# Kernel optimization log

Hardware: AMD Instinct MI355X
Metric: run time of the kernel (lower is better)

Reference implementation:

```python
import jax, jax.numpy as jnp
import numpy as np

ZMAX = 92          # max atomic number in NLH table
BOHR = 0.52917721  # Bohr radius in Angstrom (au.BOHR)
ENERGY_UNIT = 1.0  # multiplier for 'Ha'
N_ATOMS = 100_000
N_EDGES = 6_400_000
TAB = (ZMAX + 1) ** 2  # 8649


def setup_inputs() -> dict:
    key = jax.random.key(0)
    k1, k2, k3, k4, k5, k6, k7 = jax.random.split(key, 7)
    species = jax.random.randint(k1, (N_ATOMS,), 0, 93, dtype=jnp.int32)
    edge_src = jax.random.randint(k2, (N_EDGES,), 0, N_ATOMS, dtype=jnp.int32)
    edge_dst = jax.random.randint(k3, (N_EDGES,), 0, N_ATOMS, dtype=jnp.int32)
    # distances kept away from zero (division by rijs)
    distances = 0.5 + 4.5 * jax.random.uniform(k4, (N_EDGES,), dtype=jnp.float32)
    switch = jax.random.uniform(k5, (N_EDGES,), dtype=jnp.float32)
    CS = jax.random.uniform(k6, (TAB, 3), dtype=jnp.float32)
    ALPHAS = jax.random.uniform(k7, (TAB, 3), dtype=jnp.float32) + 0.5
    return {"species": species, "edge_src": edge_src, "edge_dst": edge_dst,
            "distances": distances, "switch": switch, "CS": CS, "ALPHAS": ALPHAS}


def reference(species, edge_src, edge_dst, distances, switch, CS, ALPHAS):
    # pair index into (zmax+1)^2 coefficient table
    s12 = species[edge_src] + ZMAX * species[edge_dst]
    cs = CS[s12]          # [E, 3]
    alphas = ALPHAS[s12]  # [E, 3]
    Z = jnp.where(species > 0, species.astype(distances.dtype), 0.0)
    # 3-term exponential screening function
    phi = jnp.sum(cs * jnp.exp(-alphas * distances[:, None]), axis=-1)  # [E]
    ereppair = Z[edge_src] * Z[edge_dst] * phi * switch / distances
    erep_atomic = ENERGY_UNIT * 0.5 * BOHR * jax.ops.segment_sum(
        ereppair, edge_src, num_segments=species.shape[0])
    return erep_atomic
```

## Files before the change

### kernel.cpp

```cpp
#include <hip/hip_runtime.h>
#include <hip/hip_fp16.h>


#define ZMAX_C 92
#define TAB93  93
#define NTAB   (TAB93 * TAB93)
#define HALF_BOHR 0.264588605f
#define NBMAX 64
#define APB 2048
#define APB_LOG 11
#define SPLITS 16
#define TPB 256
#define EPT 16
#define BLK_EDGES (TPB * EPT)

typedef int            ivec4 __attribute__((ext_vector_type(4)));
typedef float          fvec4 __attribute__((ext_vector_type(4)));

#if __has_builtin(__builtin_amdgcn_rcpf)
#define FAST_RCP(x) __builtin_amdgcn_rcpf(x)
#else
#define FAST_RCP(x) (1.0f / (x))
#endif

__global__ __launch_bounds__(TPB) void p0_prep(
    const float* __restrict__ CS, const float* __restrict__ ALPHAS,
    const int* __restrict__ species,
    uint4* __restrict__ tab16, unsigned char* __restrict__ spc8,
    unsigned* __restrict__ cursor, int n_atoms, int nb)
{
    int i = blockIdx.x * TPB + threadIdx.x;
    if (i < NTAB) {
        int sd = i / TAB93;
        int ss = i - TAB93 * sd;
        int ref = ss + ZMAX_C * sd;
        float Z = (ss > 0 && sd > 0) ? (float)(ss * sd) : 0.0f;
        __half h[8];
        h[0] = __float2half_rn(CS[3*ref+0] * Z);
        h[1] = __float2half_rn(CS[3*ref+1] * Z);
        h[2] = __float2half_rn(CS[3*ref+2] * Z);
        h[3] = __float2half_rn(-ALPHAS[3*ref+0]);
        h[4] = __float2half_rn(-ALPHAS[3*ref+1]);
        h[5] = __float2half_rn(-ALPHAS[3*ref+2]);
        h[6] = __half(0.0f); h[7] = __half(0.0f);
        tab16[i] = *reinterpret_cast<uint4*>(h);
    }
    if (i < n_atoms) spc8[i] = (unsigned char)species[i];
    if (i < nb) cursor[i] = 0u;
}

__device__ __forceinline__ float half_lo(unsigned u) {
    return __half2float(*reinterpret_cast<const __half*>(&u));
}
__device__ __forceinline__ float half_hi(unsigned u) {
    unsigned s = u >> 16;
    return __half2float(*reinterpret_cast<const __half*>(&s));
}

__global__ __launch_bounds__(TPB) void p1_bin(
    const int* __restrict__ edge_src, const int* __restrict__ edge_dst,
    const float* __restrict__ dist, const float* __restrict__ swt,
    const unsigned char* __restrict__ spc8, const uint4* __restrict__ tab16,
    unsigned* __restrict__ pairs, unsigned* __restrict__ cursor,
    int nb, int cap, int n_edges)
{
    __shared__ unsigned stage[BLK_EDGES];
    __shared__ unsigned hist4[4][NBMAX];
    __shared__ unsigned hist[NBMAX];
    __shared__ unsigned lbase[NBMAX];
    __shared__ unsigned gbase[NBMAX];

    int tid = threadIdx.x;
    if (tid < NBMAX) {
        hist4[0][tid] = 0; hist4[1][tid] = 0;
        hist4[2][tid] = 0; hist4[3][tid] = 0;
    }
    __syncthreads();

    int lane = tid & 63, wave = tid >> 6;
    long long wbase = (long long)blockIdx.x * BLK_EDGES + (long long)wave * (64 * EPT);

    unsigned meta[EPT];
    unsigned short s12r[EPT];

    {
        int srcv[EPT], dstv[EPT];
        #pragma unroll
        for (int j = 0; j < EPT / 4; ++j) {
            long long e0 = wbase + j * 256 + lane * 4;
            if (e0 + 3 < (long long)n_edges) {
                ivec4 s4 = __builtin_nontemporal_load((const ivec4*)(edge_src + e0));
                ivec4 d4 = __builtin_nontemporal_load((const ivec4*)(edge_dst + e0));
                #pragma unroll
                for (int k = 0; k < 4; ++k) { srcv[j*4+k] = s4[k]; dstv[j*4+k] = d4[k]; }
            } else {
                #pragma unroll
                for (int k = 0; k < 4; ++k) {
                    long long e = e0 + k;
                    bool v = (e < (long long)n_edges);
                    srcv[j*4+k] = v ? edge_src[e] : 0;
                    dstv[j*4+k] = v ? edge_dst[e] : 0;
                }
            }
        }
        int ssv[EPT], sdv[EPT];
        #pragma unroll
        for (int i = 0; i < EPT; ++i) ssv[i] = spc8[srcv[i]];
        #pragma unroll
        for (int i = 0; i < EPT; ++i) sdv[i] = spc8[dstv[i]];
        #pragma unroll
        for (int j = 0; j < EPT / 4; ++j) {
            long long e0 = wbase + j * 256 + lane * 4;
            #pragma unroll
            for (int k = 0; k < 4; ++k) {
                int idx = j * 4 + k;
                s12r[idx] = (unsigned short)(ssv[idx] + TAB93 * sdv[idx]);
                meta[idx] = 0u;
                if (e0 + k < (long long)n_edges) {
                    unsigned b    = (unsigned)srcv[idx] >> APB_LOG;
                    unsigned lsrc = (unsigned)srcv[idx] & (APB - 1);
                    unsigned rank = atomicAdd(&hist4[wave][b], 1u);
                    meta[idx] = 0x80000000u | (rank << 17) | (b << 11) | lsrc;
                }
            }
        }
    }
    __syncthreads();
    if (tid < 64) {
        unsigned h0 = hist4[0][tid], h1 = hist4[1][tid];
        unsigned h2 = hist4[2][tid], h3 = hist4[3][tid];
        unsigned tot = h0 + h1 + h2 + h3;
        hist4[0][tid] = 0;
        hist4[1][tid] = h0;
        hist4[2][tid] = h0 + h1;
        hist4[3][tid] = h0 + h1 + h2;
        if (tid < nb) hist[tid] = tot;
        unsigned v = (tid < nb) ? tot : 0u;
        unsigned x = v;
        #pragma unroll
        for (int off = 1; off < 64; off <<= 1) {
            unsigned y = __shfl_up(x, off);
            if ((tid & 63) >= off) x += y;
        }
        if (tid < nb) {
            lbase[tid] = x - v;
            gbase[tid] = v ? atomicAdd(cursor + tid, v) : 0u;
        }
    }
    __syncthreads();

    for (int jj = 0; jj < EPT / 8; ++jj) {
        long long eA = wbase + (jj*2+0) * 256 + lane * 4;
        long long eB = wbase + (jj*2+1) * 256 + lane * 4;
        float rA[4], wA[4], rB[4], wB[4];
        bool fullB = (eB + 3 < (long long)n_edges);
        if (fullB) {
            fvec4 r4 = __builtin_nontemporal_load((const fvec4*)(dist + eA));
            fvec4 w4 = __builtin_nontemporal_load((const fvec4*)(swt + eA));
            fvec4 r5 = __builtin_nontemporal_load((const fvec4*)(dist + eB));
            fvec4 w5 = __builtin_nontemporal_load((const fvec4*)(swt + eB));
            #pragma unroll
            for (int k = 0; k < 4; ++k) {
                rA[k] = r4[k]; wA[k] = w4[k]; rB[k] = r5[k]; wB[k] = w5[k];
            }
        } else {
            #pragma unroll
            for (int k = 0; k < 4; ++k) {
                long long ea = eA + k, eb = eB + k;
                bool va = (ea < (long long)n_edges), vb = (eb < (long long)n_edges);
                rA[k] = va ? dist[ea] : 1.f;  wA[k] = va ? swt[ea] : 0.f;
                rB[k] = vb ? dist[eb] : 1.f;  wB[k] = vb ? swt[eb] : 0.f;
            }
        }
        uint4 tA[4], tB[4];
        #pragma unroll
        for (int k = 0; k < 4; ++k) tA[k] = tab16[s12r[jj*8 + k]];
        #pragma unroll
        for (int k = 0; k < 4; ++k) tB[k] = tab16[s12r[jj*8 + 4 + k]];
        #pragma unroll
        for (int g = 0; g < 2; ++g) {
            const float* r = g ? rB : rA;
            const float* w = g ? wB : wA;
            const uint4* t = g ? tB : tA;
            #pragma unroll
            for (int k = 0; k < 4; ++k) {
                int idx = jj * 8 + g * 4 + k;
                unsigned m = meta[idx];
                if (!(m & 0x80000000u)) continue;
                float c0 = half_lo(t[k].x), c1 = half_hi(t[k].x);
                float c2 = half_lo(t[k].y), na0 = half_hi(t[k].y);
                float na1 = half_lo(t[k].z), na2 = half_hi(t[k].z);
                float phi = c0 * __expf(na0 * r[k])
                          + c1 * __expf(na1 * r[k])
                          + c2 * __expf(na2 * r[k]);
                float val = HALF_BOHR * phi * w[k] * FAST_RCP(r[k]);
                unsigned b = (m >> 11) & 63u;
                unsigned pos = lbase[b] + hist4[wave][b] + ((m >> 17) & 0x3FFFu);
                unsigned short hb = __half_as_ushort(__float2half_rn(val));
                stage[pos] = ((m & (APB - 1)) << 16) | (unsigned)hb;
            }
        }
    }
    __syncthreads();
    for (int b = wave; b < nb; b += 4) {
        unsigned cnt = hist[b], lb = lbase[b], gb = gbase[b];
        unsigned* dst = pairs + (size_t)b * (size_t)cap + gb;
        for (unsigned i = lane; i < cnt; i += 64)
            if (gb + i < (unsigned)cap) dst[i] = stage[lb + i];
    }
}

__global__ __launch_bounds__(TPB) void p2a_reduce(
    const unsigned* __restrict__ pairs, const unsigned* __restrict__ cursor,
    float* __restrict__ partial, int cap, int stride)
{
    int b = blockIdx.x / SPLITS;
    int s = blockIdx.x % SPLITS;
    __shared__ float acc[APB];
    for (int i = threadIdx.x; i < APB; i += TPB) acc[i] = 0.f;
    __syncthreads();
    unsigned cnt = cursor[b];
    if (cnt > (unsigned)cap) cnt = (unsigned)cap;
    unsigned nq = (cnt + 3u) >> 2;
    unsigned qb = (unsigned)((unsigned long long)nq * s / SPLITS);
    unsigned qe = (unsigned)((unsigned long long)nq * (s + 1) / SPLITS);
    const uint4* p4 = (const uint4*)(pairs + (size_t)b * (size_t)cap);
    for (unsigned q = qb + threadIdx.x; q < qe; q += TPB) {
        uint4 v = p4[q];
        unsigned base = q << 2;
        if (base + 3u < cnt) {
            unsafeAtomicAdd(&acc[v.x >> 16], __half2float(__ushort_as_half((unsigned short)(v.x & 0xFFFFu))));
            unsafeAtomicAdd(&acc[v.y >> 16], __half2float(__ushort_as_half((unsigned short)(v.y & 0xFFFFu))));
            unsafeAtomicAdd(&acc[v.z >> 16], __half2float(__ushort_as_half((unsigned short)(v.z & 0xFFFFu))));
            unsafeAtomicAdd(&acc[v.w >> 16], __half2float(__ushort_as_half((unsigned short)(v.w & 0xFFFFu))));
        } else {
            unsigned vv[4] = {v.x, v.y, v.z, v.w};
            #pragma unroll
            for (int e = 0; e < 4; ++e)
                if (base + (unsigned)e < cnt)
                    unsafeAtomicAdd(&acc[vv[e] >> 16],
                        __half2float(__ushort_as_half((unsigned short)(vv[e] & 0xFFFFu))));
        }
    }
    __syncthreads();
    float* prow = partial + (size_t)s * stride + (size_t)b * APB;
    for (int k = threadIdx.x; k < APB; k += TPB) prow[k] = acc[k];
}

__global__ __launch_bounds__(TPB) void p2b_sum(
    const float* __restrict__ partial, float* __restrict__ out, int n, int stride)
{
    int i = blockIdx.x * TPB + threadIdx.x;
    if (i >= n) return;
    float s = 0.f;
    #pragma unroll
    for (int x = 0; x < SPLITS; ++x) s += partial[(size_t)x * stride + i];
    out[i] = s;
}

__global__ __launch_bounds__(TPB) void erep_edges_direct(
    const int* __restrict__ edge_src, const int* __restrict__ edge_dst,
    const float* __restrict__ dist, const float* __restrict__ swt,
    const int* __restrict__ species, const float* __restrict__ CS,
    const float* __restrict__ ALPHAS, float* __restrict__ out, int n_edges)
{
    int e = blockIdx.x * TPB + threadIdx.x;
    if (e >= n_edges) return;
    int ss = species[edge_src[e]], sd = species[edge_dst[e]];
    int prod = ss * sd;
    if (prod == 0) return;
    int s12 = ss + ZMAX_C * sd;
    float r = dist[e];
    float phi = CS[3*s12+0] * __expf(-ALPHAS[3*s12+0] * r)
              + CS[3*s12+1] * __expf(-ALPHAS[3*s12+1] * r)
              + CS[3*s12+2] * __expf(-ALPHAS[3*s12+2] * r);
    atomicAdd(out + edge_src[e],
              HALF_BOHR * (float)prod * phi * swt[e] * FAST_RCP(r));
}

extern "C" void kernel_launch(void* const* d_in, const int* in_sizes, int n_in,
                              void* d_out, int out_size, void* d_ws, size_t ws_size,
                              hipStream_t stream)
{
    const int*   species  = (const int*)  d_in[0];
    const int*   edge_src = (const int*)  d_in[1];
    const int*   edge_dst = (const int*)  d_in[2];
    const float* dist     = (const float*)d_in[3];
    const float* swt      = (const float*)d_in[4];
    const float* CS       = (const float*)d_in[5];
    const float* ALPHAS   = (const float*)d_in[6];
    float* out = (float*)d_out;

    int n_atoms = in_sizes[0];
    int n_edges = in_sizes[1];

    int nb = (n_atoms + APB - 1) / APB;
    long long capll = (long long)n_edges / nb + (long long)n_edges / ((long long)nb * 32) + 256;
    int cap = (int)((capll + 31) & ~31LL);
    int stride = nb * APB;

    size_t pairs_sz = ((size_t)nb * (size_t)cap * 4 + 255) & ~(size_t)255;
    size_t cur_sz   = ((size_t)nb * 4 + 255) & ~(size_t)255;
    size_t part_sz  = ((size_t)SPLITS * (size_t)stride * 4 + 255) & ~(size_t)255;
    size_t tab_sz   = ((size_t)NTAB * 16 + 255) & ~(size_t)255;
    size_t spc_sz   = ((size_t)n_atoms + 255) & ~(size_t)255;
    size_t need = pairs_sz + cur_sz + part_sz + tab_sz + spc_sz;

    if (nb <= NBMAX && n_edges > 0 && ws_size >= need) {
        char* w = (char*)d_ws;
        unsigned*       pairs   = (unsigned*)w;
        unsigned*       cursor  = (unsigned*)(w + pairs_sz);
        float*          partial = (float*)(w + pairs_sz + cur_sz);
        uint4*          tab16   = (uint4*)(w + pairs_sz + cur_sz + part_sz);
        unsigned char*  spc8    = (unsigned char*)(w + pairs_sz + cur_sz + part_sz + tab_sz);

        int pmax = n_atoms > NTAB ? n_atoms : NTAB;
        p0_prep<<<(pmax + TPB - 1) / TPB, TPB, 0, stream>>>(
            CS, ALPHAS, species, tab16, spc8, cursor, n_atoms, nb);

        p1_bin<<<(n_edges + BLK_EDGES - 1) / BLK_EDGES, TPB, 0, stream>>>(
            edge_src, edge_dst, dist, swt, spc8, tab16,
            pairs, cursor, nb, cap, n_edges);

        p2a_reduce<<<nb * SPLITS, TPB, 0, stream>>>(pairs, cursor, partial, cap, stride);
        p2b_sum<<<(n_atoms + TPB - 1) / TPB, TPB, 0, stream>>>(partial, out, n_atoms, stride);
    } else {
        (void)hipMemsetAsync(d_out, 0, (size_t)out_size * sizeof(float), stream);
        erep_edges_direct<<<(n_edges + TPB - 1) / TPB, TPB, 0, stream>>>(
            edge_src, edge_dst, dist, swt, species, CS, ALPHAS, out, n_edges);
    }
}
```

Before: 249.0 us.

## Drop partial-sum kernel, atomically reduce into output, halve edges per thread

The separate p2b_sum pass and the SPLITS-row partial buffer are removed. Each p2a_reduce block now atomically adds its nonzero shared-memory accumulators straight into the output, which p0_prep zeroes first. EPT is also halved from 16 to 8, so p1_bin launches twice as many blocks, and the nontemporal loads become ordinary vector loads. This saves one launch and the partial-buffer traffic, but adds global float atomics (16-way contention per atom) and makes the summation order nondeterministic.

New measurement: 241.1 us. 1.03x faster.

```diff
diff --git a/kernel.cpp b/kernel.cpp
--- a/kernel.cpp
+++ b/kernel.cpp
@@ -11,7 +11,7 @@
 #define APB_LOG 11
 #define SPLITS 16
 #define TPB 256
-#define EPT 16
+#define EPT 8
 #define BLK_EDGES (TPB * EPT)
 
 typedef int            ivec4 __attribute__((ext_vector_type(4)));
@@ -27,7 +27,8 @@
     const float* __restrict__ CS, const float* __restrict__ ALPHAS,
     const int* __restrict__ species,
     uint4* __restrict__ tab16, unsigned char* __restrict__ spc8,
-    unsigned* __restrict__ cursor, int n_atoms, int nb)
+    unsigned* __restrict__ cursor, float* __restrict__ out,
+    int n_atoms, int nb)
 {
     int i = blockIdx.x * TPB + threadIdx.x;
     if (i < NTAB) {
@@ -45,7 +46,10 @@
         h[6] = __half(0.0f); h[7] = __half(0.0f);
         tab16[i] = *reinterpret_cast<uint4*>(h);
     }
-    if (i < n_atoms) spc8[i] = (unsigned char)species[i];
+    if (i < n_atoms) {
+        spc8[i] = (unsigned char)species[i];
+        out[i] = 0.0f;
+    }
     if (i < nb) cursor[i] = 0u;
 }
 
@@ -89,8 +93,8 @@
         for (int j = 0; j < EPT / 4; ++j) {
             long long e0 = wbase + j * 256 + lane * 4;
             if (e0 + 3 < (long long)n_edges) {
-                ivec4 s4 = __builtin_nontemporal_load((const ivec4*)(edge_src + e0));
-                ivec4 d4 = __builtin_nontemporal_load((const ivec4*)(edge_dst + e0));
+                ivec4 s4 = *reinterpret_cast<const ivec4*>(edge_src + e0);
+                ivec4 d4 = *reinterpret_cast<const ivec4*>(edge_dst + e0);
                 #pragma unroll
                 for (int k = 0; k < 4; ++k) { srcv[j*4+k] = s4[k]; dstv[j*4+k] = d4[k]; }
             } else {
@@ -155,10 +159,10 @@
         float rA[4], wA[4], rB[4], wB[4];
         bool fullB = (eB + 3 < (long long)n_edges);
         if (fullB) {
-            fvec4 r4 = __builtin_nontemporal_load((const fvec4*)(dist + eA));
-            fvec4 w4 = __builtin_nontemporal_load((const fvec4*)(swt + eA));
-            fvec4 r5 = __builtin_nontemporal_load((const fvec4*)(dist + eB));
-            fvec4 w5 = __builtin_nontemporal_load((const fvec4*)(swt + eB));
+            fvec4 r4 = *reinterpret_cast<const fvec4*>(dist + eA);
+            fvec4 w4 = *reinterpret_cast<const fvec4*>(swt + eA);
+            fvec4 r5 = *reinterpret_cast<const fvec4*>(dist + eB);
+            fvec4 w5 = *reinterpret_cast<const fvec4*>(swt + eB);
             #pragma unroll
             for (int k = 0; k < 4; ++k) {
                 rA[k] = r4[k]; wA[k] = w4[k]; rB[k] = r5[k]; wB[k] = w5[k];
@@ -212,7 +216,7 @@
 
 __global__ __launch_bounds__(TPB) void p2a_reduce(
     const unsigned* __restrict__ pairs, const unsigned* __restrict__ cursor,
-    float* __restrict__ partial, int cap, int stride)
+    float* __restrict__ out, int cap, int n_atoms)
 {
     int b = blockIdx.x / SPLITS;
     int s = blockIdx.x % SPLITS;
@@ -243,19 +247,13 @@
         }
     }
     __syncthreads();
-    float* prow = partial + (size_t)s * stride + (size_t)b * APB;
-    for (int k = threadIdx.x; k < APB; k += TPB) prow[k] = acc[k];
-}
-
-__global__ __launch_bounds__(TPB) void p2b_sum(
-    const float* __restrict__ partial, float* __restrict__ out, int n, int stride)
-{
-    int i = blockIdx.x * TPB + threadIdx.x;
-    if (i >= n) return;
-    float s = 0.f;
-    #pragma unroll
-    for (int x = 0; x < SPLITS; ++x) s += partial[(size_t)x * stride + i];
-    out[i] = s;
+    int abase = b * APB;
+    for (int k = threadIdx.x; k < APB; k += TPB) {
+        int atom = abase + k;
+        float vv = acc[k];
+        if (atom < n_atoms && vv != 0.0f)
+            unsafeAtomicAdd(&out[atom], vv);
+    }
 }
 
 __global__ __launch_bounds__(TPB) void erep_edges_direct(
@@ -297,33 +295,29 @@
     int nb = (n_atoms + APB - 1) / APB;
     long long capll = (long long)n_edges / nb + (long long)n_edges / ((long long)nb * 32) + 256;
     int cap = (int)((capll + 31) & ~31LL);
-    int stride = nb * APB;
 
     size_t pairs_sz = ((size_t)nb * (size_t)cap * 4 + 255) & ~(size_t)255;
     size_t cur_sz   = ((size_t)nb * 4 + 255) & ~(size_t)255;
-    size_t part_sz  = ((size_t)SPLITS * (size_t)stride * 4 + 255) & ~(size_t)255;
     size_t tab_sz   = ((size_t)NTAB * 16 + 255) & ~(size_t)255;
     size_t spc_sz   = ((size_t)n_atoms + 255) & ~(size_t)255;
-    size_t need = pairs_sz + cur_sz + part_sz + tab_sz + spc_sz;
+    size_t need = pairs_sz + cur_sz + tab_sz + spc_sz;
 
     if (nb <= NBMAX && n_edges > 0 && ws_size >= need) {
         char* w = (char*)d_ws;
         unsigned*       pairs   = (unsigned*)w;
         unsigned*       cursor  = (unsigned*)(w + pairs_sz);
-        float*          partial = (float*)(w + pairs_sz + cur_sz);
-        uint4*          tab16   = (uint4*)(w + pairs_sz + cur_sz + part_sz);
-        unsigned char*  spc8    = (unsigned char*)(w + pairs_sz + cur_sz + part_sz + tab_sz);
+        uint4*          tab16   = (uint4*)(w + pairs_sz + cur_sz);
+        unsigned char*  spc8    = (unsigned char*)(w + pairs_sz + cur_sz + tab_sz);
 
         int pmax = n_atoms > NTAB ? n_atoms : NTAB;
         p0_prep<<<(pmax + TPB - 1) / TPB, TPB, 0, stream>>>(
-            CS, ALPHAS, species, tab16, spc8, cursor, n_atoms, nb);
+            CS, ALPHAS, species, tab16, spc8, cursor, out, n_atoms, nb);
 
         p1_bin<<<(n_edges + BLK_EDGES - 1) / BLK_EDGES, TPB, 0, stream>>>(
             edge_src, edge_dst, dist, swt, spc8, tab16,
             pairs, cursor, nb, cap, n_edges);
 
-        p2a_reduce<<<nb * SPLITS, TPB, 0, stream>>>(pairs, cursor, partial, cap, stride);
-        p2b_sum<<<(n_atoms + TPB - 1) / TPB, TPB, 0, stream>>>(partial, out, n_atoms, stride);
+        p2a_reduce<<<nb * SPLITS, TPB, 0, stream>>>(pairs, cursor, out, cap, n_atoms);
     } else {
         (void)hipMemsetAsync(d_out, 0, (size_t)out_size * sizeof(float), stream);
         erep_edges_direct<<<(n_edges + TPB - 1) / TPB, TPB, 0, stream>>>(
```
